# Kernel tuning notes

Measured on AMD Instinct MI355X. Metric: run time of the kernel, lower is better.

The kernel has to match this reference:

```python
import jax, jax.numpy as jnp
import numpy as np

H = 8       # heads
D = 512     # hidden_size
DH = D // H # head dim
FF = 2048   # hardcoded FFN hidden in source


def _layernorm(x, g, b, eps=1e-5):
    mu = jnp.mean(x, axis=-1, keepdims=True)
    var = jnp.var(x, axis=-1, keepdims=True)
    return (x - mu) * jax.lax.rsqrt(var + eps) * g + b


def setup_inputs() -> dict:
    key = jax.random.key(0)
    ks = jax.random.split(key, 12)
    B, S = 2, 4096
    s = lambda fan_in: 1.0 / np.sqrt(fan_in)
    return {
        "reaction": jax.random.normal(ks[0], (B, S, D), dtype=jnp.float32),
        "mask": jnp.ones((B, 1, 1, S), dtype=jnp.int32),
        # attention weights stored as [in, out] (torch Linear weight.T)
        "Wq": jax.random.uniform(ks[1], (D, D), jnp.float32, -s(D), s(D)),
        "Wk": jax.random.uniform(ks[2], (D, D), jnp.float32, -s(D), s(D)),
        "Wv": jax.random.uniform(ks[3], (D, D), jnp.float32, -s(D), s(D)),
        "Wo": jax.random.uniform(ks[4], (D, D), jnp.float32, -s(D), s(D)),
        "bo": jnp.zeros((D,), jnp.float32),
        "W1": jax.random.uniform(ks[5], (D, FF), jnp.float32, -s(D), s(D)),
        "b1": jnp.zeros((FF,), jnp.float32),
        "W2": jax.random.uniform(ks[6], (FF, D), jnp.float32, -s(FF), s(FF)),
        "b2": jnp.zeros((D,), jnp.float32),
        "g_sa": jnp.ones((D,), jnp.float32),
        "b_sa": jnp.zeros((D,), jnp.float32),
        "g_ff": jnp.ones((D,), jnp.float32),
        "b_ff": jnp.zeros((D,), jnp.float32),
    }


def reference(reaction, mask, Wq, Wk, Wv, Wo, bo, W1, b1, W2, b2, g_sa, b_sa, g_ff, b_ff):
    B, S, _ = reaction.shape
    # --- self-attention part (pre-norm) ---
    x = _layernorm(reaction, g_sa, b_sa)
    q = (x @ Wq).reshape(B, S, H, DH)
    k = (x @ Wk).reshape(B, S, H, DH)
    v = (x @ Wv).reshape(B, S, H, DH)
    scale = DH ** (-0.5)
    scores = jnp.einsum('bqhd,bkhd->bhqk', q * scale, k)  # [B,H,S,S]
    scores = jnp.where(mask == 0, -jnp.inf, scores)
    att = jax.nn.softmax(scores, axis=-1)
    ctx = jnp.einsum('bhqk,bkhd->bqhd', att, v).reshape(B, S, D)
    attn_out = jax.nn.gelu(ctx @ Wo + bo, approximate=False)  # GELU after output proj (as in source)
    x = attn_out + reaction
    # --- feed-forward part (pre-norm) ---
    y = _layernorm(x, g_ff, b_ff)
    y = jax.nn.gelu(y @ W1 + b1, approximate=False) @ W2 + b2
    return y + x
```

## Files before the change

### kernel.cpp

```cpp
#include <hip/hip_runtime.h>
#include <hip/hip_bf16.h>
#include <math.h>

#define HN 8
#define DM 512
#define DHD 64
#define FFD 2048
#define BB 2
#define SS 4096
#define MT (BB*SS)

typedef __bf16 bf16_t;
typedef __bf16 bf16x8 __attribute__((ext_vector_type(8)));
typedef __bf16 bf16x4 __attribute__((ext_vector_type(4)));
typedef float  floatx4 __attribute__((ext_vector_type(4)));

__device__ __forceinline__ void async_copy16(const bf16_t* g, bf16_t* l) {
  __builtin_amdgcn_global_load_lds((const __attribute__((address_space(1))) void*)g,
                                   (__attribute__((address_space(3))) void*)l,
                                   16, 0, 0);
}

#if __has_builtin(__builtin_amdgcn_exp2f)
__device__ __forceinline__ float fast_exp2(float x) { return __builtin_amdgcn_exp2f(x); }
#else
__device__ __forceinline__ float fast_exp2(float x) { return __expf(x * 0.69314718056f); }
#endif

__device__ __forceinline__ float gelu_f(float x) {
  float y = 0.7978845608f * (x + 0.044715f * x * x * x);
  float e = fast_exp2(y * 2.885390082f);
  float th = 1.0f - 2.0f / (e + 1.0f);
  return 0.5f * x * (1.0f + th);
}

__global__ __launch_bounds__(256)
void prep_ln(const float* __restrict__ x, const float* __restrict__ g,
             const float* __restrict__ be, bf16_t* __restrict__ out,
             const float* __restrict__ Wq, const float* __restrict__ Wk,
             const float* __restrict__ Wv, const float* __restrict__ Wo,
             const float* __restrict__ W1, const float* __restrict__ W2,
             bf16_t* __restrict__ WqkvT, bf16_t* __restrict__ WoT,
             bf16_t* __restrict__ W1T, bf16_t* __restrict__ W2T)
{
  __shared__ float tile[32][33];
  if (blockIdx.x < 2048) {
    const int wave = threadIdx.x >> 6, lane = threadIdx.x & 63;
    const int row = blockIdx.x * 4 + wave;
    const float* xr = x + (size_t)row * DM + lane * 8;
    float4 a = *(const float4*)xr;
    float4 c = *(const float4*)(xr + 4);
    float s  = (a.x + a.y) + (a.z + a.w) + (c.x + c.y) + (c.z + c.w);
    float s2 = (a.x*a.x + a.y*a.y) + (a.z*a.z + a.w*a.w)
             + (c.x*c.x + c.y*c.y) + (c.z*c.z + c.w*c.w);
#pragma unroll
    for (int o = 1; o < 64; o <<= 1) { s += __shfl_xor(s, o); s2 += __shfl_xor(s2, o); }
    const float mu = s * (1.0f / DM);
    const float rv = rsqrtf(s2 * (1.0f / DM) - mu * mu + 1e-5f);
    float4 g0 = *(const float4*)(g + lane * 8);
    float4 g1 = *(const float4*)(g + lane * 8 + 4);
    float4 b0 = *(const float4*)(be + lane * 8);
    float4 b1 = *(const float4*)(be + lane * 8 + 4);
    bf16x8 o8;
    o8[0] = (bf16_t)((a.x - mu) * rv * g0.x + b0.x);
    o8[1] = (bf16_t)((a.y - mu) * rv * g0.y + b0.y);
    o8[2] = (bf16_t)((a.z - mu) * rv * g0.z + b0.z);
    o8[3] = (bf16_t)((a.w - mu) * rv * g0.w + b0.w);
    o8[4] = (bf16_t)((c.x - mu) * rv * g1.x + b1.x);
    o8[5] = (bf16_t)((c.y - mu) * rv * g1.y + b1.y);
    o8[6] = (bf16_t)((c.z - mu) * rv * g1.z + b1.z);
    o8[7] = (bf16_t)((c.w - mu) * rv * g1.w + b1.w);
    *(bf16x8*)(out + (size_t)row * DM + lane * 8) = o8;
    return;
  }
  const int bid = blockIdx.x - 2048;
  const float* src; bf16_t* dst; int Kd, Nd, n0, k0;
  if (bid < 768) {
    int seg = bid >> 8, t = bid & 255;
    src = (seg == 0) ? Wq : (seg == 1) ? Wk : Wv;
    dst = WqkvT + (size_t)seg * 512 * 512;
    Kd = 512; Nd = 512; n0 = (t & 15) * 32; k0 = (t >> 4) * 32;
  } else if (bid < 1024) {
    int t = bid - 768; src = Wo; dst = WoT;
    Kd = 512; Nd = 512; n0 = (t & 15) * 32; k0 = (t >> 4) * 32;
  } else if (bid < 2048) {
    int t = bid - 1024; src = W1; dst = W1T;
    Kd = 512; Nd = 2048; n0 = (t & 63) * 32; k0 = (t >> 6) * 32;
  } else {
    int t = bid - 2048; src = W2; dst = W2T;
    Kd = 2048; Nd = 512; n0 = (t & 15) * 32; k0 = (t >> 4) * 32;
  }
  const int tx = threadIdx.x & 31, ty = threadIdx.x >> 5;
#pragma unroll
  for (int i = 0; i < 32; i += 8)
    tile[ty + i][tx] = src[(size_t)(k0 + ty + i) * Nd + n0 + tx];
  __syncthreads();
#pragma unroll
  for (int i = 0; i < 32; i += 8)
    dst[(size_t)(n0 + ty + i) * Kd + k0 + tx] = (bf16_t)tile[tx][ty + i];
}

__global__ __launch_bounds__(256)
void ln_kernel(const float* __restrict__ x, const float* __restrict__ g,
               const float* __restrict__ be, bf16_t* __restrict__ out)
{
  const int wave = threadIdx.x >> 6, lane = threadIdx.x & 63;
  const int row = blockIdx.x * 4 + wave;
  const float* xr = x + (size_t)row * DM + lane * 8;
  float4 a = *(const float4*)xr;
  float4 c = *(const float4*)(xr + 4);
  float s  = (a.x + a.y) + (a.z + a.w) + (c.x + c.y) + (c.z + c.w);
  float s2 = (a.x*a.x + a.y*a.y) + (a.z*a.z + a.w*a.w)
           + (c.x*c.x + c.y*c.y) + (c.z*c.z + c.w*c.w);
#pragma unroll
  for (int o = 1; o < 64; o <<= 1) { s += __shfl_xor(s, o); s2 += __shfl_xor(s2, o); }
  const float mu = s * (1.0f / DM);
  const float rv = rsqrtf(s2 * (1.0f / DM) - mu * mu + 1e-5f);
  float4 g0 = *(const float4*)(g + lane * 8);
  float4 g1 = *(const float4*)(g + lane * 8 + 4);
  float4 b0 = *(const float4*)(be + lane * 8);
  float4 b1 = *(const float4*)(be + lane * 8 + 4);
  bf16x8 o8;
  o8[0] = (bf16_t)((a.x - mu) * rv * g0.x + b0.x);
  o8[1] = (bf16_t)((a.y - mu) * rv * g0.y + b0.y);
  o8[2] = (bf16_t)((a.z - mu) * rv * g0.z + b0.z);
  o8[3] = (bf16_t)((a.w - mu) * rv * g0.w + b0.w);
  o8[4] = (bf16_t)((c.x - mu) * rv * g1.x + b1.x);
  o8[5] = (bf16_t)((c.y - mu) * rv * g1.y + b1.y);
  o8[6] = (bf16_t)((c.z - mu) * rv * g1.z + b1.z);
  o8[7] = (bf16_t)((c.w - mu) * rv * g1.w + b1.w);
  *(bf16x8*)(out + (size_t)row * DM + lane * 8) = o8;
}

template <int MI, int NJ, int EPI, int BKT = 64>
__global__ __launch_bounds__(256)
void gemm_bt(const bf16_t* __restrict__ A, const bf16_t* __restrict__ Bt,
             const int M, const int N, const int K,
             const float* __restrict__ bias, const float* __restrict__ res,
             bf16_t* __restrict__ outb, float* __restrict__ outf,
             bf16_t* __restrict__ out2, bf16_t* __restrict__ out3, const int ldt)
{
  constexpr int MTILE = 32 * MI, NTILE = 32 * NJ;
  constexpr int CH = BKT / 8;
  constexpr int ACOPY = MTILE * BKT / 2048;
  constexpr int BCOPY = NTILE * BKT / 2048;
  __shared__ __align__(16) bf16_t lA[MTILE * BKT];
  __shared__ __align__(16) bf16_t lB[NTILE * BKT];
  const int tid = threadIdx.x;
  const int wave = tid >> 6, lane = tid & 63;
  const int wm = wave & 1, wn = wave >> 1;
  const int quad = lane >> 4, l16 = lane & 15;

  int srA[ACOPY > BCOPY ? ACOPY : BCOPY], scA[ACOPY > BCOPY ? ACOPY : BCOPY];
#pragma unroll
  for (int i = 0; i < (ACOPY > BCOPY ? ACOPY : BCOPY); ++i) {
    int flat = tid + 256 * i;
    int r = flat / CH, ch = flat % CH;
    srA[i] = r;
    scA[i] = (ch ^ (r & (CH - 1))) * 8;
  }
  const bf16_t* Ab = A + (size_t)(blockIdx.x * MTILE) * K;
  const bf16_t* Bb = Bt + (size_t)(blockIdx.y * NTILE) * K;

  const floatx4 vzero = {0.f, 0.f, 0.f, 0.f};
  floatx4 acc[MI][NJ];
#pragma unroll
  for (int i = 0; i < MI; ++i)
#pragma unroll
    for (int j = 0; j < NJ; ++j) acc[i][j] = vzero;

  for (int k0 = 0; k0 < K; k0 += BKT) {
    __syncthreads();
#pragma unroll
    for (int i = 0; i < ACOPY; ++i)
      async_copy16(Ab + (size_t)srA[i] * K + k0 + scA[i], lA + (tid + 256 * i) * 8);
#pragma unroll
    for (int i = 0; i < BCOPY; ++i)
      async_copy16(Bb + (size_t)srA[i] * K + k0 + scA[i], lB + (tid + 256 * i) * 8);
    __syncthreads();
#pragma unroll
    for (int c = 0; c < BKT / 32; ++c) {
      bf16x8 af[MI], bfv[NJ];
#pragma unroll
      for (int i = 0; i < MI; ++i)
        af[i] = *(const bf16x8*)(lA + (wm * 16 * MI + i * 16 + l16) * BKT
                                 + (((c * 4 + quad) ^ (l16 & (CH - 1))) * 8));
#pragma unroll
      for (int j = 0; j < NJ; ++j)
        bfv[j] = *(const bf16x8*)(lB + (wn * 16 * NJ + j * 16 + l16) * BKT
                                  + (((c * 4 + quad) ^ (l16 & (CH - 1))) * 8));
#pragma unroll
      for (int i = 0; i < MI; ++i)
#pragma unroll
        for (int j = 0; j < NJ; ++j)
          acc[i][j] = __builtin_amdgcn_mfma_f32_16x16x32_bf16(af[i], bfv[j], acc[i][j], 0, 0, 0);
    }
  }

  const int m00 = blockIdx.x * MTILE + wm * 16 * MI;
  const int n00 = blockIdx.y * NTILE + wn * 16 * NJ;
#pragma unroll
  for (int i = 0; i < MI; ++i) {
#pragma unroll
    for (int j = 0; j < NJ; ++j) {
      const int m0 = m00 + i * 16 + quad * 4;
      const int n  = n00 + j * 16 + l16;
      floatx4 v = acc[i][j];
      if (EPI == 2) {
        const float bb = bias[n];
#pragma unroll
        for (int r = 0; r < 4; ++r)
          outf[(size_t)(m0 + r) * N + n] = gelu_f(v[r] + bb) + res[(size_t)(m0 + r) * N + n];
      } else if (EPI == 3) {
        const float bb = bias[n];
#pragma unroll
        for (int r = 0; r < 4; ++r)
          outb[(size_t)(m0 + r) * N + n] = (bf16_t)gelu_f(v[r] + bb);
      } else if (EPI == 4) {
        const float bb = bias[n];
#pragma unroll
        for (int r = 0; r < 4; ++r)
          outf[(size_t)(m0 + r) * N + n] = v[r] + bb + res[(size_t)(m0 + r) * N + n];
      } else {
        const int seg = blockIdx.y >> 2;
        if (seg == 0) {
#pragma unroll
          for (int r = 0; r < 4; ++r)
            outb[(size_t)(m0 + r) * 512 + n] = (bf16_t)(v[r] * 0.180336879f);
        } else if (seg == 1) {
#pragma unroll
          for (int r = 0; r < 4; ++r) out2[(size_t)(m0 + r) * 512 + (n - 512)] = (bf16_t)v[r];
        } else {
          const int o = m0 & 31;
          const int p0 = (m0 & ~31) + ((o >> 2) & 3) * 8 + ((o >> 4) << 2);
          bf16x4 pk = {(bf16_t)v[0], (bf16_t)v[1], (bf16_t)v[2], (bf16_t)v[3]};
          *(bf16x4*)(out3 + (size_t)(n - 1024) * ldt + p0) = pk;
        }
      }
    }
  }
}

__global__ __launch_bounds__(256, 2)
void attn_kernel(const bf16_t* __restrict__ qm, const bf16_t* __restrict__ km,
                 const bf16_t* __restrict__ vtm, const int* __restrict__ mask,
                 bf16_t* __restrict__ ctx)
{
  const int flat = blockIdx.x + 32 * (blockIdx.y + 8 * blockIdx.z);
  const int swz = (flat & 7) * 64 + (flat >> 3);
  const int b = swz >> 8, h = (swz >> 5) & 7;
  const int q0 = (swz & 31) * 128;
  const int tid = threadIdx.x;
  const int wave = tid >> 6, lane = tid & 63;
  const int quad = lane >> 4, l16 = lane & 15;

  __shared__ __align__(16) bf16_t lK[2][128 * DHD];
  __shared__ __align__(16) bf16_t lV[2][DHD * 128];
  __shared__ int sclean[4];

  const int* maskb = mask + b * SS;

  unsigned um = 0xFFFFFFFFu;
#pragma unroll
  for (int i = 0; i < 4; ++i) {
    int4 m = *(const int4*)(maskb + tid * 16 + i * 4);
    um = min(um, min(min((unsigned)m.x, (unsigned)m.y), min((unsigned)m.z, (unsigned)m.w)));
  }
#pragma unroll
  for (int o = 1; o < 64; o <<= 1) um = min(um, (unsigned)__shfl_xor((int)um, o));
  if (lane == 0) sclean[wave] = (int)um;
  __syncthreads();
  const bool clean = (min(min((unsigned)sclean[0], (unsigned)sclean[1]),
                          min((unsigned)sclean[2], (unsigned)sclean[3])) != 0u);

  const size_t qrow0 = (size_t)b * SS + q0;
  bf16x8 qa[2][2];
#pragma unroll
  for (int mb = 0; mb < 2; ++mb)
#pragma unroll
    for (int cc = 0; cc < 2; ++cc)
      qa[mb][cc] = *(const bf16x8*)(qm + (qrow0 + wave * 32 + mb * 16 + l16) * DM
                                    + h * DHD + cc * 32 + quad * 8);

  const floatx4 vzero = {0.f, 0.f, 0.f, 0.f};
  floatx4 cacc[2][4];
  float lsum[2] = {0.f, 0.f};
#pragma unroll
  for (int mb = 0; mb < 2; ++mb)
#pragma unroll
    for (int nb = 0; nb < 4; ++nb) cacc[mb][nb] = vzero;

  const bf16_t* Kb = km + (size_t)b * SS * DM + h * DHD;
  const bf16_t* Vb = vtm + (size_t)(h * DHD) * MT + (size_t)b * SS;

  const bf16_t* pk[4]; const bf16_t* pv[4];
#pragma unroll
  for (int i = 0; i < 4; ++i) {
    int p = tid + 256 * i;
    int key = p >> 3, cs = (p & 7) ^ (key & 7);
    pk[i] = Kb + (size_t)key * DM + cs * 8;
    int dh = p >> 4, cs2 = (p & 15) ^ (dh & 7);
    pv[i] = Vb + (size_t)dh * MT + cs2 * 8;
  }

  auto stage = [&](int buf, int s0) {
#pragma unroll
    for (int i = 0; i < 4; ++i) {
      int p8 = (tid + 256 * i) * 8;
      async_copy16(pk[i] + (size_t)s0 * DM, lK[buf] + p8);
      async_copy16(pv[i] + s0, lV[buf] + p8);
    }
  };

  auto exp_pv = [&](floatx4 sa[2], floatx4 sb[2], const bf16x8 av[4]) {
    bf16x8 pf[2];
#pragma unroll
    for (int mb = 0; mb < 2; ++mb) {
      float e0 = fast_exp2(sa[mb][0]), e1 = fast_exp2(sa[mb][1]);
      float e2 = fast_exp2(sa[mb][2]), e3 = fast_exp2(sa[mb][3]);
      float e4 = fast_exp2(sb[mb][0]), e5 = fast_exp2(sb[mb][1]);
      float e6 = fast_exp2(sb[mb][2]), e7 = fast_exp2(sb[mb][3]);
      lsum[mb] += ((e0 + e1) + (e2 + e3)) + ((e4 + e5) + (e6 + e7));
      pf[mb][0] = (bf16_t)e0; pf[mb][1] = (bf16_t)e1;
      pf[mb][2] = (bf16_t)e2; pf[mb][3] = (bf16_t)e3;
      pf[mb][4] = (bf16_t)e4; pf[mb][5] = (bf16_t)e5;
      pf[mb][6] = (bf16_t)e6; pf[mb][7] = (bf16_t)e7;
    }
    __builtin_amdgcn_s_setprio(1);
#pragma unroll
    for (int nb = 0; nb < 4; ++nb) {
      cacc[0][nb] = __builtin_amdgcn_mfma_f32_16x16x32_bf16(av[nb], pf[0], cacc[0][nb], 0, 0, 0);
      cacc[1][nb] = __builtin_amdgcn_mfma_f32_16x16x32_bf16(av[nb], pf[1], cacc[1][nb], 0, 0, 0);
    }
    __builtin_amdgcn_s_setprio(0);
  };

  if (clean) {
    auto compute_clean = [&](const bf16_t* __restrict__ lKb,
                             const bf16_t* __restrict__ lVb) {
      bf16x8 kf[2][2][2];
      bf16x8 av[2][4];
#pragma unroll
      for (int cc = 0; cc < 2; ++cc) {
        const int ko = ((cc * 4 + quad) ^ (l16 & 7)) * 8;
        kf[0][cc][0] = *(const bf16x8*)(lKb + (l16) * 64 + ko);
        kf[0][cc][1] = *(const bf16x8*)(lKb + (16 + l16) * 64 + ko);
      }
#pragma unroll
      for (int nb = 0; nb < 4; ++nb)
        av[0][nb] = *(const bf16x8*)(lVb + (nb * 16 + l16) * 128
                                     + ((quad ^ (l16 & 7)) * 8));
#pragma unroll
      for (int c = 0; c < 4; ++c) {
        const int buf = c & 1, nbuf = buf ^ 1;
        floatx4 sa[2], sb[2];
        sa[0] = vzero; sa[1] = vzero; sb[0] = vzero; sb[1] = vzero;
        __builtin_amdgcn_s_setprio(1);
#pragma unroll
        for (int cc = 0; cc < 2; ++cc)
#pragma unroll
          for (int mb = 0; mb < 2; ++mb) {
            sa[mb] = __builtin_amdgcn_mfma_f32_16x16x32_bf16(kf[buf][cc][0], qa[mb][cc], sa[mb], 0, 0, 0);
            sb[mb] = __builtin_amdgcn_mfma_f32_16x16x32_bf16(kf[buf][cc][1], qa[mb][cc], sb[mb], 0, 0, 0);
          }
        __builtin_amdgcn_s_setprio(0);
        if (c < 3) {
#pragma unroll
          for (int cc = 0; cc < 2; ++cc) {
            const int ko = (((cc * 4 + quad)) ^ (l16 & 7)) * 8;
            kf[nbuf][cc][0] = *(const bf16x8*)(lKb + ((c + 1) * 32 + l16) * 64 + ko);
            kf[nbuf][cc][1] = *(const bf16x8*)(lKb + ((c + 1) * 32 + 16 + l16) * 64 + ko);
          }
          const int chn = ((c + 1) * 4 + quad) ^ (l16 & 7);
#pragma unroll
          for (int nb = 0; nb < 4; ++nb)
            av[nbuf][nb] = *(const bf16x8*)(lVb + (nb * 16 + l16) * 128 + chn * 8);
        }
        exp_pv(sa, sb, av[buf]);
      }
    };

    stage(0, 0);
#pragma unroll 1
    for (int s0 = 0; s0 < SS; s0 += 256) {
      __syncthreads();
      stage(1, s0 + 128);
      compute_clean(lK[0], lV[0]);
      __syncthreads();
      if (s0 + 256 < SS) stage(0, s0 + 256);
      compute_clean(lK[1], lV[1]);
    }
  } else {
    auto compute_masked = [&](const bf16_t* __restrict__ lKb,
                              const bf16_t* __restrict__ lVb, int s0) {
#pragma unroll
      for (int c = 0; c < 4; ++c) {
        floatx4 sa[2], sb[2];
        sa[0] = vzero; sa[1] = vzero; sb[0] = vzero; sb[1] = vzero;
#pragma unroll
        for (int cc = 0; cc < 2; ++cc) {
          const int ko = ((cc * 4 + quad) ^ (l16 & 7)) * 8;
          bf16x8 kf0 = *(const bf16x8*)(lKb + (c * 32 + l16) * 64 + ko);
          bf16x8 kf1 = *(const bf16x8*)(lKb + (c * 32 + 16 + l16) * 64 + ko);
          __builtin_amdgcn_s_setprio(1);
#pragma unroll
          for (int mb = 0; mb < 2; ++mb) {
            sa[mb] = __builtin_amdgcn_mfma_f32_16x16x32_bf16(kf0, qa[mb][cc], sa[mb], 0, 0, 0);
            sb[mb] = __builtin_amdgcn_mfma_f32_16x16x32_bf16(kf1, qa[mb][cc], sb[mb], 0, 0, 0);
          }
          __builtin_amdgcn_s_setprio(0);
        }
        const int4 m0 = *(const int4*)(maskb + s0 + c * 32 + quad * 4);
        const int4 m1 = *(const int4*)(maskb + s0 + c * 32 + 16 + quad * 4);
#pragma unroll
        for (int mb = 0; mb < 2; ++mb) {
          if (m0.x == 0) sa[mb][0] = -1e30f;
          if (m0.y == 0) sa[mb][1] = -1e30f;
          if (m0.z == 0) sa[mb][2] = -1e30f;
          if (m0.w == 0) sa[mb][3] = -1e30f;
          if (m1.x == 0) sb[mb][0] = -1e30f;
          if (m1.y == 0) sb[mb][1] = -1e30f;
          if (m1.z == 0) sb[mb][2] = -1e30f;
          if (m1.w == 0) sb[mb][3] = -1e30f;
        }
        const int ch = (c * 4 + quad) ^ (l16 & 7);
        bf16x8 av[4];
#pragma unroll
        for (int nb = 0; nb < 4; ++nb)
          av[nb] = *(const bf16x8*)(lVb + (nb * 16 + l16) * 128 + ch * 8);
        exp_pv(sa, sb, av);
      }
    };

    stage(0, 0);
#pragma unroll 1
    for (int s0 = 0; s0 < SS; s0 += 256) {
      __syncthreads();
      stage(1, s0 + 128);
      compute_masked(lK[0], lV[0], s0);
      __syncthreads();
      if (s0 + 256 < SS) stage(0, s0 + 256);
      compute_masked(lK[1], lV[1], s0 + 128);
    }
  }

#pragma unroll
  for (int mb = 0; mb < 2; ++mb) {
    float tot = lsum[mb];
    tot += __shfl_xor(tot, 16);
    tot += __shfl_xor(tot, 32);
    const float inv = 1.0f / tot;
    const size_t qrow = qrow0 + wave * 32 + mb * 16 + l16;
#pragma unroll
    for (int nb = 0; nb < 4; ++nb) {
      bf16x4 o = {(bf16_t)(cacc[mb][nb][0] * inv), (bf16_t)(cacc[mb][nb][1] * inv),
                  (bf16_t)(cacc[mb][nb][2] * inv), (bf16_t)(cacc[mb][nb][3] * inv)};
      *(bf16x4*)(ctx + qrow * DM + h * DHD + nb * 16 + quad * 4) = o;
    }
  }
}

extern "C" void kernel_launch(void* const* d_in, const int* in_sizes, int n_in,
                              void* d_out, int out_size, void* d_ws, size_t ws_size,
                              hipStream_t stream)
{
  (void)in_sizes; (void)n_in; (void)out_size; (void)ws_size;
  const float* reaction = (const float*)d_in[0];
  const int*   mask     = (const int*)d_in[1];
  const float* Wq = (const float*)d_in[2];
  const float* Wk = (const float*)d_in[3];
  const float* Wv = (const float*)d_in[4];
  const float* Wo = (const float*)d_in[5];
  const float* bo = (const float*)d_in[6];
  const float* W1 = (const float*)d_in[7];
  const float* b1 = (const float*)d_in[8];
  const float* W2 = (const float*)d_in[9];
  const float* b2 = (const float*)d_in[10];
  const float* g_sa = (const float*)d_in[11];
  const float* b_sa = (const float*)d_in[12];
  const float* g_ff = (const float*)d_in[13];
  const float* b_ff = (const float*)d_in[14];
  float* out = (float*)d_out;

  char* ws = (char*)d_ws;
  size_t off = 0;
  auto take = [&](size_t bytes) -> char* {
    char* p = ws + off;
    off += (bytes + 255) & ~(size_t)255;
    return p;
  };

  bf16_t* xln   = (bf16_t*)take((size_t)MT * DM * 2);
  bf16_t* WqkvT = (bf16_t*)take((size_t)3 * DM * DM * 2);
  bf16_t* WoT   = (bf16_t*)take((size_t)DM * DM * 2);
  bf16_t* W1T   = (bf16_t*)take((size_t)FFD * DM * 2);
  bf16_t* W2T   = (bf16_t*)take((size_t)DM * FFD * 2);
  bf16_t* qb    = (bf16_t*)take((size_t)MT * DM * 2);
  bf16_t* kb    = (bf16_t*)take((size_t)MT * DM * 2);
  bf16_t* vtb   = (bf16_t*)take((size_t)DM * MT * 2);
  bf16_t* ctx   = (bf16_t*)take((size_t)MT * DM * 2);
  float*  x2    = (float*)take((size_t)MT * DM * 4);
  bf16_t* yb    = xln;
  bf16_t* hb    = qb;

  prep_ln<<<5120, 256, 0, stream>>>(reaction, g_sa, b_sa, xln,
                                    Wq, Wk, Wv, Wo, W1, W2, WqkvT, WoT, W1T, W2T);

  gemm_bt<4, 4, 5><<<dim3(64, 12), 256, 0, stream>>>(xln, WqkvT, MT, 3 * DM, DM,
                                                     nullptr, nullptr, qb, nullptr, kb, vtb, MT);

  attn_kernel<<<dim3(SS / 128, HN, BB), 256, 0, stream>>>(qb, kb, vtb, mask, ctx);

  gemm_bt<4, 2, 2><<<dim3(64, 8), 256, 0, stream>>>(ctx, WoT, MT, DM, DM,
                                                    bo, reaction, nullptr, x2, nullptr, nullptr, 0);

  ln_kernel<<<MT / 4, 256, 0, stream>>>(x2, g_ff, b_ff, yb);
  gemm_bt<4, 4, 3><<<dim3(64, 16), 256, 0, stream>>>(yb, W1T, MT, FFD, DM,
                                                     b1, nullptr, hb, nullptr, nullptr, nullptr, 0);
  gemm_bt<4, 2, 4, 128><<<dim3(64, 8), 256, 0, stream>>>(hb, W2T, MT, DM, FFD,
                                                         b2, x2, nullptr, out, nullptr, nullptr, 0);
}
```

Baseline: 267.9 us.

## Software-pipeline QK^T with exp/PV in attention and drop setprio hints

```diff
diff --git a/kernel.cpp b/kernel.cpp
--- a/kernel.cpp
+++ b/kernel.cpp
@@ -326,13 +326,11 @@
       pf[mb][4] = (bf16_t)e4; pf[mb][5] = (bf16_t)e5;
       pf[mb][6] = (bf16_t)e6; pf[mb][7] = (bf16_t)e7;
     }
-    __builtin_amdgcn_s_setprio(1);
 #pragma unroll
     for (int nb = 0; nb < 4; ++nb) {
       cacc[0][nb] = __builtin_amdgcn_mfma_f32_16x16x32_bf16(av[nb], pf[0], cacc[0][nb], 0, 0, 0);
       cacc[1][nb] = __builtin_amdgcn_mfma_f32_16x16x32_bf16(av[nb], pf[1], cacc[1][nb], 0, 0, 0);
     }
-    __builtin_amdgcn_s_setprio(0);
   };
 
   if (clean) {
@@ -350,24 +348,22 @@
       for (int nb = 0; nb < 4; ++nb)
         av[0][nb] = *(const bf16x8*)(lVb + (nb * 16 + l16) * 128
                                      + ((quad ^ (l16 & 7)) * 8));
+      floatx4 sa_c[2], sb_c[2];
+      sa_c[0] = vzero; sa_c[1] = vzero; sb_c[0] = vzero; sb_c[1] = vzero;
+#pragma unroll
+      for (int cc = 0; cc < 2; ++cc)
+#pragma unroll
+        for (int mb = 0; mb < 2; ++mb) {
+          sa_c[mb] = __builtin_amdgcn_mfma_f32_16x16x32_bf16(kf[0][cc][0], qa[mb][cc], sa_c[mb], 0, 0, 0);
+          sb_c[mb] = __builtin_amdgcn_mfma_f32_16x16x32_bf16(kf[0][cc][1], qa[mb][cc], sb_c[mb], 0, 0, 0);
+        }
 #pragma unroll
       for (int c = 0; c < 4; ++c) {
         const int buf = c & 1, nbuf = buf ^ 1;
-        floatx4 sa[2], sb[2];
-        sa[0] = vzero; sa[1] = vzero; sb[0] = vzero; sb[1] = vzero;
-        __builtin_amdgcn_s_setprio(1);
-#pragma unroll
-        for (int cc = 0; cc < 2; ++cc)
-#pragma unroll
-          for (int mb = 0; mb < 2; ++mb) {
-            sa[mb] = __builtin_amdgcn_mfma_f32_16x16x32_bf16(kf[buf][cc][0], qa[mb][cc], sa[mb], 0, 0, 0);
-            sb[mb] = __builtin_amdgcn_mfma_f32_16x16x32_bf16(kf[buf][cc][1], qa[mb][cc], sb[mb], 0, 0, 0);
-          }
-        __builtin_amdgcn_s_setprio(0);
         if (c < 3) {
 #pragma unroll
           for (int cc = 0; cc < 2; ++cc) {
-            const int ko = (((cc * 4 + quad)) ^ (l16 & 7)) * 8;
+            const int ko = ((cc * 4 + quad) ^ (l16 & 7)) * 8;
             kf[nbuf][cc][0] = *(const bf16x8*)(lKb + ((c + 1) * 32 + l16) * 64 + ko);
             kf[nbuf][cc][1] = *(const bf16x8*)(lKb + ((c + 1) * 32 + 16 + l16) * 64 + ko);
           }
@@ -376,7 +372,37 @@
           for (int nb = 0; nb < 4; ++nb)
             av[nbuf][nb] = *(const bf16x8*)(lVb + (nb * 16 + l16) * 128 + chn * 8);
         }
-        exp_pv(sa, sb, av[buf]);
+        bf16x8 pf[2];
+#pragma unroll
+        for (int mb = 0; mb < 2; ++mb) {
+          float e0 = fast_exp2(sa_c[mb][0]), e1 = fast_exp2(sa_c[mb][1]);
+          float e2 = fast_exp2(sa_c[mb][2]), e3 = fast_exp2(sa_c[mb][3]);
+          float e4 = fast_exp2(sb_c[mb][0]), e5 = fast_exp2(sb_c[mb][1]);
+          float e6 = fast_exp2(sb_c[mb][2]), e7 = fast_exp2(sb_c[mb][3]);
+          lsum[mb] += ((e0 + e1) + (e2 + e3)) + ((e4 + e5) + (e6 + e7));
+          pf[mb][0] = (bf16_t)e0; pf[mb][1] = (bf16_t)e1;
+          pf[mb][2] = (bf16_t)e2; pf[mb][3] = (bf16_t)e3;
+          pf[mb][4] = (bf16_t)e4; pf[mb][5] = (bf16_t)e5;
+          pf[mb][6] = (bf16_t)e6; pf[mb][7] = (bf16_t)e7;
+        }
+        floatx4 sa_n[2], sb_n[2];
+        sa_n[0] = vzero; sa_n[1] = vzero; sb_n[0] = vzero; sb_n[1] = vzero;
+        if (c < 3) {
+#pragma unroll
+          for (int cc = 0; cc < 2; ++cc)
+#pragma unroll
+            for (int mb = 0; mb < 2; ++mb) {
+              sa_n[mb] = __builtin_amdgcn_mfma_f32_16x16x32_bf16(kf[nbuf][cc][0], qa[mb][cc], sa_n[mb], 0, 0, 0);
+              sb_n[mb] = __builtin_amdgcn_mfma_f32_16x16x32_bf16(kf[nbuf][cc][1], qa[mb][cc], sb_n[mb], 0, 0, 0);
+            }
+        }
+#pragma unroll
+        for (int nb = 0; nb < 4; ++nb) {
+          cacc[0][nb] = __builtin_amdgcn_mfma_f32_16x16x32_bf16(av[buf][nb], pf[0], cacc[0][nb], 0, 0, 0);
+          cacc[1][nb] = __builtin_amdgcn_mfma_f32_16x16x32_bf16(av[buf][nb], pf[1], cacc[1][nb], 0, 0, 0);
+        }
+#pragma unroll
+        for (int mb = 0; mb < 2; ++mb) { sa_c[mb] = sa_n[mb]; sb_c[mb] = sb_n[mb]; }
       }
     };
 
@@ -402,13 +428,11 @@
           const int ko = ((cc * 4 + quad) ^ (l16 & 7)) * 8;
           bf16x8 kf0 = *(const bf16x8*)(lKb + (c * 32 + l16) * 64 + ko);
           bf16x8 kf1 = *(const bf16x8*)(lKb + (c * 32 + 16 + l16) * 64 + ko);
-          __builtin_amdgcn_s_setprio(1);
 #pragma unroll
           for (int mb = 0; mb < 2; ++mb) {
             sa[mb] = __builtin_amdgcn_mfma_f32_16x16x32_bf16(kf0, qa[mb][cc], sa[mb], 0, 0, 0);
             sb[mb] = __builtin_amdgcn_mfma_f32_16x16x32_bf16(kf1, qa[mb][cc], sb[mb], 0, 0, 0);
           }
-          __builtin_amdgcn_s_setprio(0);
         }
         const int4 m0 = *(const int4*)(maskb + s0 + c * 32 + quad * 4);
         const int4 m1 = *(const int4*)(maskb + s0 + c * 32 + 16 + quad * 4);
@@ -511,8 +535,8 @@
 
   attn_kernel<<<dim3(SS / 128, HN, BB), 256, 0, stream>>>(qb, kb, vtb, mask, ctx);
 
-  gemm_bt<4, 2, 2><<<dim3(64, 8), 256, 0, stream>>>(ctx, WoT, MT, DM, DM,
-                                                    bo, reaction, nullptr, x2, nullptr, nullptr, 0);
+  gemm_bt<4, 2, 2, 128><<<dim3(64, 8), 256, 0, stream>>>(ctx, WoT, MT, DM, DM,
+                                                         bo, reaction, nullptr, x2, nullptr, nullptr, 0);
 
   ln_kernel<<<MT / 4, 256, 0, stream>>>(x2, g_ff, b_ff, yb);
   gemm_bt<4, 4, 3><<<dim3(64, 16), 256, 0, stream>>>(yb, W1T, MT, FFD, DM,
```

Result: slower. 273.5 us (+2.1%).
